# Kernel optimization log

Measured on AMD Instinct MI355X. Metric: run time of the kernel, lower is better.

The kernel has to match this reference:

```python
import jax, jax.numpy as jnp
import numpy as np

N_NODES = 100000
N_EDGES = 1600000
N_GRAPHS = 1024
D = 128
L = 3
BN_EPS = 1e-5


def setup_inputs() -> dict:
    key = jax.random.key(0)
    ks = jax.random.split(key, 16)
    x = jax.random.normal(ks[0], (N_NODES, D), dtype=jnp.float32)
    edge_index = jax.random.randint(ks[1], (2, N_EDGES), 0, N_NODES, dtype=jnp.int64)
    batch = jnp.sort(jax.random.randint(ks[2], (N_NODES,), 0, N_GRAPHS, dtype=jnp.int64))
    w = lambda k, shape: jax.random.normal(k, shape, dtype=jnp.float32) * 0.05
    return {
        "x": x,
        "edge_index": edge_index,
        "batch": batch,
        "conv_W1": w(ks[3], (L, D, D)),
        "conv_b1": w(ks[4], (L, D)),
        "bn_gamma": jax.random.uniform(ks[5], (L, D), dtype=jnp.float32) + 0.5,
        "bn_beta": w(ks[6], (L, D)),
        "bn_mean": w(ks[7], (L, D)),
        "bn_var": jax.random.uniform(ks[8], (L, D), dtype=jnp.float32) + 0.5,
        "conv_W2": w(ks[9], (L, D, D)),
        "conv_b2": w(ks[10], (L, D)),
        "head_W1": w(ks[11], (D, D)),
        "head_b1": w(ks[12], (D,)),
        "head_W2": w(ks[13], (D, D)),
        "head_b2": w(ks[14], (D,)),
    }


def reference(x, edge_index, batch, conv_W1, conv_b1, bn_gamma, bn_beta,
              bn_mean, bn_var, conv_W2, conv_b2, head_W1, head_b1,
              head_W2, head_b2):
    n = x.shape[0]
    src, dst = edge_index[0], edge_index[1]
    for l in range(L):
        # GINConv, eps=0: nn(x + sum_{j->i} x_j)
        agg = jax.ops.segment_sum(x[src], dst, num_segments=n)  # [N, D]
        h = x + agg
        # MLP([in, h, h]): Linear -> BatchNorm(eval) -> ReLU -> Linear
        h = h @ conv_W1[l] + conv_b1[l]
        h = (h - bn_mean[l]) * jax.lax.rsqrt(bn_var[l] + BN_EPS) * bn_gamma[l] + bn_beta[l]
        h = jax.nn.relu(h)
        h = h @ conv_W2[l] + conv_b2[l]
        x = jax.nn.relu(h)  # .relu() in the outer forward
    # global_add_pool over graph ids
    g = jax.ops.segment_sum(x, batch, num_segments=N_GRAPHS)  # [B, D]
    # head MLP (norm=None, dropout inactive at eval): Linear -> ReLU -> Linear
    g = jax.nn.relu(g @ head_W1 + head_b1)
    return g @ head_W2 + head_b2
```

## Files before the change

### kernel.cpp

```cpp
#include <hip/hip_runtime.h>

#define N_NODES  100000
#define N_EDGES  1600000
#define N_GRAPHS 1024
#define D        128
#define BN_EPS   1e-5f

#define FNSLICE      98
#define FSLICE_NODES 1024
#define FSLICE_CAP   20480
#define QCAP         96
#define CCHUNK       4000
#define CGRID        400

#define CVT_BLOCKS   6250
#define PW_BLOCKS    384
#define FOLD_BLOCKS  3
#define PZ_BLOCKS    128
#define PZ_BASE      (CVT_BLOCKS + PW_BLOCKS + FOLD_BLOCKS)
#define MISC_BASE    (PZ_BASE + PZ_BLOCKS)
#define COMPACT_BASE (MISC_BASE + 1)
#define SETUP_GRID   (COMPACT_BASE + CGRID)

#define GATHER_GRID  12500

typedef short bf16x8 __attribute__((ext_vector_type(8)));
typedef float f32x4  __attribute__((ext_vector_type(4)));

__device__ __forceinline__ ushort f2bf(float f) {
    unsigned int b = __float_as_uint(f);
    return (ushort)((b + 0x7fffu + ((b >> 16) & 1u)) >> 16);
}
__device__ __forceinline__ float bflo(unsigned int u) { return __uint_as_float(u << 16); }
__device__ __forceinline__ float bfhi(unsigned int u) { return __uint_as_float(u & 0xffff0000u); }
__device__ __forceinline__ unsigned int packbf(float x, float y) {
    return (unsigned int)f2bf(x) | ((unsigned int)f2bf(y) << 16);
}

__global__ __launch_bounds__(256) void setup_kernel(
        const float* __restrict__ x, ushort* __restrict__ xb,
        const float* __restrict__ W1, const float* __restrict__ W2,
        ushort* __restrict__ Wt,
        const float* __restrict__ b1, const float* __restrict__ gamma,
        const float* __restrict__ beta, const float* __restrict__ mean,
        const float* __restrict__ var, const float* __restrict__ b2,
        float* __restrict__ folds, float* __restrict__ pool,
        int* __restrict__ slice_tail, int* __restrict__ offsets,
        const int* __restrict__ src, const int* __restrict__ dst,
        unsigned int* __restrict__ squeue) {
    __shared__ unsigned int qbuf[FNSLICE * QCAP];
    __shared__ int qcnt[FNSLICE];
    __shared__ int qbase[FNSLICE];
    int b = blockIdx.x, t = threadIdx.x;
    if (b < CVT_BLOCKS) {
        size_t i = ((size_t)b * 256 + t) * 8;
        float4 v0 = *(const float4*)(x + i);
        float4 v1 = *(const float4*)(x + i + 4);
        uint4 o;
        o.x = packbf(v0.x, v0.y); o.y = packbf(v0.z, v0.w);
        o.z = packbf(v1.x, v1.y); o.w = packbf(v1.z, v1.w);
        *(uint4*)(xb + i) = o;
    } else if (b < CVT_BLOCKS + PW_BLOCKS) {
        int idx = (b - CVT_BLOCKS) * 256 + t;
        int i = idx >> 14, r = idx & 16383;
        int n = r >> 7, k = r & 127, l = i >> 1;
        const float* W = (i & 1) ? (W2 + (size_t)l * D * D) : (W1 + (size_t)l * D * D);
        Wt[idx] = f2bf(W[k * D + n]);
    } else if (b < PZ_BASE) {
        int idx = (b - CVT_BLOCKS - PW_BLOCKS) * 256 + t;
        if (idx < 6 * D) {
            int i = idx >> 7, j = idx & 127, l = i >> 1;
            float s, o;
            if ((i & 1) == 0) {
                float sv = gamma[l * D + j] * rsqrtf(var[l * D + j] + BN_EPS);
                s = sv;
                o = (b1[l * D + j] - mean[l * D + j]) * sv + beta[l * D + j];
            } else {
                s = 1.0f;
                o = b2[l * D + j];
            }
            folds[(size_t)i * 2 * D + j]     = s;
            folds[(size_t)i * 2 * D + D + j] = o;
        }
    } else if (b < MISC_BASE) {
        int idx = (b - PZ_BASE) * 256 + t;
        ((float4*)pool)[idx] = float4{0.f, 0.f, 0.f, 0.f};
    } else if (b == MISC_BASE) {
        if (t == 255) offsets[N_NODES] = N_EDGES;
    } else {
        for (int i = t; i < FNSLICE; i += 256) qcnt[i] = 0;
        __syncthreads();
        int e0 = (b - COMPACT_BASE) * CCHUNK;
        int eend = e0 + CCHUNK; if (eend > N_EDGES) eend = N_EDGES;
        for (int e = e0 + t; e < eend; e += 256) {
            int d = dst[e], s = src[e];
            int sl = d >> 10;
            unsigned int pk = ((unsigned int)(d & 1023) << 17) | (unsigned int)s;
            int pos = atomicAdd(&qcnt[sl], 1);
            if (pos < QCAP) qbuf[sl * QCAP + pos] = pk;
            else {
                int gp = atomicAdd(&slice_tail[sl], 1);
                squeue[(size_t)sl * FSLICE_CAP + gp] = pk;
            }
        }
        __syncthreads();
        for (int i = t; i < FNSLICE; i += 256) {
            int n = qcnt[i]; if (n > QCAP) n = QCAP;
            qbase[i] = atomicAdd(&slice_tail[i], n);
        }
        __syncthreads();
        int wv = t >> 6, ln = t & 63;
        for (int sl = wv; sl < FNSLICE; sl += 4) {
            int n = qcnt[sl]; if (n > QCAP) n = QCAP;
            int gb = qbase[sl];
            for (int i = ln; i < n; i += 64)
                squeue[(size_t)sl * FSLICE_CAP + gb + i] = qbuf[sl * QCAP + i];
        }
    }
}

__global__ __launch_bounds__(1024) void fill_local(const unsigned int* __restrict__ squeue,
                                                   const int* __restrict__ slice_tail,
                                                   int* __restrict__ offsets,
                                                   int* __restrict__ csr_src) {
    __shared__ int hist[FSLICE_NODES];
    __shared__ int cur[FSLICE_NODES];
    __shared__ int sbase[128];
    __shared__ int wsum[16];
    int sl = blockIdx.x, t = threadIdx.x;
    int n = slice_tail[sl];
    if (t < 128) sbase[t] = (t < FNSLICE) ? slice_tail[t] : 0;
    hist[t] = 0;
    __syncthreads();
    for (int off = 1; off < 128; off <<= 1) {
        int u = (t < 128 && t >= off) ? sbase[t - off] : 0;
        __syncthreads();
        if (t < 128) sbase[t] += u;
        __syncthreads();
    }
    int gbase = (sl == 0) ? 0 : sbase[sl - 1];
    size_t qb = (size_t)sl * FSLICE_CAP;
    for (int i = t; i < n; i += 1024)
        atomicAdd(&hist[squeue[qb + i] >> 17], 1);
    __syncthreads();
    int c = hist[t];
    int lane = t & 63, w = t >> 6;
    int sc = c;
#pragma unroll
    for (int off = 1; off < 64; off <<= 1) {
        int u = __shfl_up(sc, off, 64);
        if (lane >= off) sc += u;
    }
    if (lane == 63) wsum[w] = sc;
    __syncthreads();
    if (t < 16) {
        int ws = wsum[t];
        int s2 = ws;
#pragma unroll
        for (int off = 1; off < 16; off <<= 1) {
            int u = __shfl_up(s2, off, 16);
            if (t >= off) s2 += u;
        }
        wsum[t] = s2 - ws;
    }
    __syncthreads();
    int gslot = gbase + sc + wsum[w] - c;
    cur[t] = gslot;
    int node = sl * FSLICE_NODES + t;
    if (node < N_NODES) offsets[node] = gslot;
    __syncthreads();
    for (int i = t; i < n; i += 1024) {
        unsigned int p = squeue[qb + i];
        int slot = atomicAdd(&cur[p >> 17], 1);
        csr_src[slot] = (int)(p & 0x1FFFFu);
    }
}

__device__ __forceinline__ void drain_stream(const unsigned int* __restrict__ base,
                                             const int* __restrict__ csr,
                                             int i, int e, int lane,
                                             float& ax, float& ay) {
    for (; i + 15 < e; i += 16) {
        int s0 = csr[i],      s1 = csr[i + 1],  s2 = csr[i + 2],  s3 = csr[i + 3];
        int s4 = csr[i + 4],  s5 = csr[i + 5],  s6 = csr[i + 6],  s7 = csr[i + 7];
        int s8 = csr[i + 8],  s9 = csr[i + 9],  sa = csr[i + 10], sb = csr[i + 11];
        int sc = csr[i + 12], sd = csr[i + 13], se = csr[i + 14], sf = csr[i + 15];
        unsigned int v0 = base[(size_t)s0 * 64 + lane];
        unsigned int v1 = base[(size_t)s1 * 64 + lane];
        unsigned int v2 = base[(size_t)s2 * 64 + lane];
        unsigned int v3 = base[(size_t)s3 * 64 + lane];
        unsigned int v4 = base[(size_t)s4 * 64 + lane];
        unsigned int v5 = base[(size_t)s5 * 64 + lane];
        unsigned int v6 = base[(size_t)s6 * 64 + lane];
        unsigned int v7 = base[(size_t)s7 * 64 + lane];
        unsigned int v8 = base[(size_t)s8 * 64 + lane];
        unsigned int v9 = base[(size_t)s9 * 64 + lane];
        unsigned int va = base[(size_t)sa * 64 + lane];
        unsigned int vb = base[(size_t)sb * 64 + lane];
        unsigned int vc = base[(size_t)sc * 64 + lane];
        unsigned int vd = base[(size_t)sd * 64 + lane];
        unsigned int ve = base[(size_t)se * 64 + lane];
        unsigned int vf = base[(size_t)sf * 64 + lane];
        ax += bflo(v0) + bflo(v1) + bflo(v2) + bflo(v3)
            + bflo(v4) + bflo(v5) + bflo(v6) + bflo(v7)
            + bflo(v8) + bflo(v9) + bflo(va) + bflo(vb)
            + bflo(vc) + bflo(vd) + bflo(ve) + bflo(vf);
        ay += bfhi(v0) + bfhi(v1) + bfhi(v2) + bfhi(v3)
            + bfhi(v4) + bfhi(v5) + bfhi(v6) + bfhi(v7)
            + bfhi(v8) + bfhi(v9) + bfhi(va) + bfhi(vb)
            + bfhi(vc) + bfhi(vd) + bfhi(ve) + bfhi(vf);
    }
    for (; i + 3 < e; i += 4) {
        int s0 = csr[i], s1 = csr[i + 1], s2 = csr[i + 2], s3 = csr[i + 3];
        unsigned int v0 = base[(size_t)s0 * 64 + lane];
        unsigned int v1 = base[(size_t)s1 * 64 + lane];
        unsigned int v2 = base[(size_t)s2 * 64 + lane];
        unsigned int v3 = base[(size_t)s3 * 64 + lane];
        ax += bflo(v0) + bflo(v1) + bflo(v2) + bflo(v3);
        ay += bfhi(v0) + bfhi(v1) + bfhi(v2) + bfhi(v3);
    }
    for (; i < e; ++i) {
        unsigned int v = base[(size_t)csr[i] * 64 + lane];
        ax += bflo(v); ay += bfhi(v);
    }
}

__global__ __launch_bounds__(256) void gather_bf16(const ushort* __restrict__ xb,
                                                   const int* __restrict__ offsets,
                                                   const int* __restrict__ csr_src,
                                                   ushort* __restrict__ hb) {
    int wv = threadIdx.x >> 6, lane = threadIdx.x & 63;
    int n0 = (blockIdx.x * 4 + wv) * 2;
    const unsigned int* base = (const unsigned int*)xb;
    unsigned int u0 = base[(size_t)n0 * 64 + lane];
    unsigned int u1 = base[(size_t)(n0 + 1) * 64 + lane];
    float ax0 = bflo(u0), ay0 = bfhi(u0);
    float ax1 = bflo(u1), ay1 = bfhi(u1);
    int i0 = offsets[n0];
    int e0 = offsets[n0 + 1];
    int i1 = e0;
    int e1 = offsets[n0 + 2];
    while (i0 + 7 < e0 && i1 + 7 < e1) {
        int s0 = csr_src[i0],     s1 = csr_src[i0 + 1],
            s2 = csr_src[i0 + 2], s3 = csr_src[i0 + 3];
        int s4 = csr_src[i0 + 4], s5 = csr_src[i0 + 5],
            s6 = csr_src[i0 + 6], s7 = csr_src[i0 + 7];
        int r0 = csr_src[i1],     r1 = csr_src[i1 + 1],
            r2 = csr_src[i1 + 2], r3 = csr_src[i1 + 3];
        int r4 = csr_src[i1 + 4], r5 = csr_src[i1 + 5],
            r6 = csr_src[i1 + 6], r7 = csr_src[i1 + 7];
        unsigned int v0 = base[(size_t)s0 * 64 + lane];
        unsigned int v1 = base[(size_t)s1 * 64 + lane];
        unsigned int v2 = base[(size_t)s2 * 64 + lane];
        unsigned int v3 = base[(size_t)s3 * 64 + lane];
        unsigned int v4 = base[(size_t)s4 * 64 + lane];
        unsigned int v5 = base[(size_t)s5 * 64 + lane];
        unsigned int v6 = base[(size_t)s6 * 64 + lane];
        unsigned int v7 = base[(size_t)s7 * 64 + lane];
        unsigned int w0 = base[(size_t)r0 * 64 + lane];
        unsigned int w1 = base[(size_t)r1 * 64 + lane];
        unsigned int w2 = base[(size_t)r2 * 64 + lane];
        unsigned int w3 = base[(size_t)r3 * 64 + lane];
        unsigned int w4 = base[(size_t)r4 * 64 + lane];
        unsigned int w5 = base[(size_t)r5 * 64 + lane];
        unsigned int w6 = base[(size_t)r6 * 64 + lane];
        unsigned int w7 = base[(size_t)r7 * 64 + lane];
        ax0 += bflo(v0) + bflo(v1) + bflo(v2) + bflo(v3)
             + bflo(v4) + bflo(v5) + bflo(v6) + bflo(v7);
        ay0 += bfhi(v0) + bfhi(v1) + bfhi(v2) + bfhi(v3)
             + bfhi(v4) + bfhi(v5) + bfhi(v6) + bfhi(v7);
        ax1 += bflo(w0) + bflo(w1) + bflo(w2) + bflo(w3)
             + bflo(w4) + bflo(w5) + bflo(w6) + bflo(w7);
        ay1 += bfhi(w0) + bfhi(w1) + bfhi(w2) + bfhi(w3)
             + bfhi(w4) + bfhi(w5) + bfhi(w6) + bfhi(w7);
        i0 += 8; i1 += 8;
    }
    drain_stream(base, csr_src, i0, e0, lane, ax0, ay0);
    drain_stream(base, csr_src, i1, e1, lane, ax1, ay1);
    ((unsigned int*)hb)[(size_t)n0 * 64 + lane]       = packbf(ax0, ay0);
    ((unsigned int*)hb)[(size_t)(n0 + 1) * 64 + lane] = packbf(ax1, ay1);
}

__global__ __launch_bounds__(512, 4) void fused_gemm(const ushort* __restrict__ in,
                                                     ushort* __restrict__ out,
                                                     const ushort* __restrict__ Wt1,
                                                     const ushort* __restrict__ Wt2,
                                                     const float* __restrict__ fold1,
                                                     const float* __restrict__ fold2) {
    __shared__ ushort As[128 * 136];
    __shared__ ushort Bs[128 * 136];
    int t = threadIdx.x;
    int row0 = blockIdx.x * 128;

#pragma unroll
    for (int i = 0; i < 4; ++i) {
        int f = t + 512 * i; int m = f >> 4, g = f & 15;
        *(float4*)(As + m * 136 + g * 8) = *(const float4*)(in + (size_t)(row0 + m) * D + g * 8);
        *(float4*)(Bs + m * 136 + g * 8) = *(const float4*)(Wt1 + (size_t)m * D + g * 8);
    }
    const uint4* w2v = (const uint4*)Wt2;
    uint4 p0 = w2v[t];
    uint4 p1 = w2v[t + 512];
    uint4 p2 = w2v[t + 1024];
    uint4 p3 = w2v[t + 1536];
    __syncthreads();

    int lane = t & 63, wv = t >> 6;
    int quad = lane >> 4, mr = lane & 15;
    int mbase = wv * 16;
    const ushort* ap = As + (mbase + mr) * 136 + quad * 8;
    bf16x8 a0 = *(const bf16x8*)(ap);
    bf16x8 a1 = *(const bf16x8*)(ap + 32);
    bf16x8 a2 = *(const bf16x8*)(ap + 64);
    bf16x8 a3 = *(const bf16x8*)(ap + 96);

#pragma unroll
    for (int nt = 0; nt < 8; ++nt) {
        const ushort* bq = Bs + (nt * 16 + mr) * 136 + quad * 8;
        bf16x8 b0 = *(const bf16x8*)(bq);
        bf16x8 b1 = *(const bf16x8*)(bq + 32);
        bf16x8 b2 = *(const bf16x8*)(bq + 64);
        bf16x8 b3 = *(const bf16x8*)(bq + 96);
        f32x4 acc = {0.f, 0.f, 0.f, 0.f};
        acc = __builtin_amdgcn_mfma_f32_16x16x32_bf16(a0, b0, acc, 0, 0, 0);
        acc = __builtin_amdgcn_mfma_f32_16x16x32_bf16(a1, b1, acc, 0, 0, 0);
        acc = __builtin_amdgcn_mfma_f32_16x16x32_bf16(a2, b2, acc, 0, 0, 0);
        acc = __builtin_amdgcn_mfma_f32_16x16x32_bf16(a3, b3, acc, 0, 0, 0);
        int j = nt * 16 + mr;
        float s = fold1[j], o = fold1[D + j];
#pragma unroll
        for (int r = 0; r < 4; ++r) {
            float z = fmaxf(fmaf(acc[r], s, o), 0.0f);
            As[(mbase + quad * 4 + r) * 136 + j] = f2bf(z);
        }
    }
    __syncthreads();

    {
        int f0 = t;          *(uint4*)(Bs + (f0 >> 4) * 136 + (f0 & 15) * 8) = p0;
        int f1 = t + 512;    *(uint4*)(Bs + (f1 >> 4) * 136 + (f1 & 15) * 8) = p1;
        int f2 = t + 1024;   *(uint4*)(Bs + (f2 >> 4) * 136 + (f2 & 15) * 8) = p2;
        int f3 = t + 1536;   *(uint4*)(Bs + (f3 >> 4) * 136 + (f3 & 15) * 8) = p3;
    }
    const ushort* hp = As + (mbase + mr) * 136 + quad * 8;
    bf16x8 h0 = *(const bf16x8*)(hp);
    bf16x8 h1 = *(const bf16x8*)(hp + 32);
    bf16x8 h2 = *(const bf16x8*)(hp + 64);
    bf16x8 h3 = *(const bf16x8*)(hp + 96);
    __syncthreads();

#pragma unroll
    for (int nt = 0; nt < 8; ++nt) {
        const ushort* bq = Bs + (nt * 16 + mr) * 136 + quad * 8;
        bf16x8 b0 = *(const bf16x8*)(bq);
        bf16x8 b1 = *(const bf16x8*)(bq + 32);
        bf16x8 b2 = *(const bf16x8*)(bq + 64);
        bf16x8 b3 = *(const bf16x8*)(bq + 96);
        f32x4 acc = {0.f, 0.f, 0.f, 0.f};
        acc = __builtin_amdgcn_mfma_f32_16x16x32_bf16(h0, b0, acc, 0, 0, 0);
        acc = __builtin_amdgcn_mfma_f32_16x16x32_bf16(h1, b1, acc, 0, 0, 0);
        acc = __builtin_amdgcn_mfma_f32_16x16x32_bf16(h2, b2, acc, 0, 0, 0);
        acc = __builtin_amdgcn_mfma_f32_16x16x32_bf16(h3, b3, acc, 0, 0, 0);
        int j = nt * 16 + mr;
        float o = fold2[D + j];
#pragma unroll
        for (int r = 0; r < 4; ++r) {
            float z = fmaxf(acc[r] + o, 0.0f);
            As[(mbase + quad * 4 + r) * 136 + j] = f2bf(z);
        }
    }
    __syncthreads();

#pragma unroll
    for (int i = 0; i < 8; ++i) {
        int f = t + 512 * i; int lr = f >> 5, g = f & 31;
        if (row0 + lr < N_NODES)
            *(float2*)(out + (size_t)(row0 + lr) * D + g * 4) =
                *(const float2*)(As + lr * 136 + g * 4);
    }
}

__global__ __launch_bounds__(512, 4) void fused_gemm_pool(const ushort* __restrict__ in,
                                                          const int* __restrict__ batch,
                                                          float* __restrict__ pool,
                                                          const ushort* __restrict__ Wt1,
                                                          const ushort* __restrict__ Wt2,
                                                          const float* __restrict__ fold1,
                                                          const float* __restrict__ fold2) {
    __shared__ ushort As[128 * 136];
    __shared__ ushort Bs[128 * 136];
    __shared__ int bb[128];
    int t = threadIdx.x;
    int row0 = blockIdx.x * 128;

#pragma unroll
    for (int i = 0; i < 4; ++i) {
        int f = t + 512 * i; int m = f >> 4, g = f & 15;
        *(float4*)(As + m * 136 + g * 8) = *(const float4*)(in + (size_t)(row0 + m) * D + g * 8);
        *(float4*)(Bs + m * 136 + g * 8) = *(const float4*)(Wt1 + (size_t)m * D + g * 8);
    }
    const uint4* w2v = (const uint4*)Wt2;
    uint4 p0 = w2v[t];
    uint4 p1 = w2v[t + 512];
    uint4 p2 = w2v[t + 1024];
    uint4 p3 = w2v[t + 1536];
    __syncthreads();

    int lane = t & 63, wv = t >> 6;
    int quad = lane >> 4, mr = lane & 15;
    int mbase = wv * 16;
    const ushort* ap = As + (mbase + mr) * 136 + quad * 8;
    bf16x8 a0 = *(const bf16x8*)(ap);
    bf16x8 a1 = *(const bf16x8*)(ap + 32);
    bf16x8 a2 = *(const bf16x8*)(ap + 64);
    bf16x8 a3 = *(const bf16x8*)(ap + 96);

#pragma unroll
    for (int nt = 0; nt < 8; ++nt) {
        const ushort* bq = Bs + (nt * 16 + mr) * 136 + quad * 8;
        bf16x8 b0 = *(const bf16x8*)(bq);
        bf16x8 b1 = *(const bf16x8*)(bq + 32);
        bf16x8 b2 = *(const bf16x8*)(bq + 64);
        bf16x8 b3 = *(const bf16x8*)(bq + 96);
        f32x4 acc = {0.f, 0.f, 0.f, 0.f};
        acc = __builtin_amdgcn_mfma_f32_16x16x32_bf16(a0, b0, acc, 0, 0, 0);
        acc = __builtin_amdgcn_mfma_f32_16x16x32_bf16(a1, b1, acc, 0, 0, 0);
        acc = __builtin_amdgcn_mfma_f32_16x16x32_bf16(a2, b2, acc, 0, 0, 0);
        acc = __builtin_amdgcn_mfma_f32_16x16x32_bf16(a3, b3, acc, 0, 0, 0);
        int j = nt * 16 + mr;
        float s = fold1[j], o = fold1[D + j];
#pragma unroll
        for (int r = 0; r < 4; ++r) {
            float z = fmaxf(fmaf(acc[r], s, o), 0.0f);
            As[(mbase + quad * 4 + r) * 136 + j] = f2bf(z);
        }
    }
    __syncthreads();

    {
        int f0 = t;          *(uint4*)(Bs + (f0 >> 4) * 136 + (f0 & 15) * 8) = p0;
        int f1 = t + 512;    *(uint4*)(Bs + (f1 >> 4) * 136 + (f1 & 15) * 8) = p1;
        int f2 = t + 1024;   *(uint4*)(Bs + (f2 >> 4) * 136 + (f2 & 15) * 8) = p2;
        int f3 = t + 1536;   *(uint4*)(Bs + (f3 >> 4) * 136 + (f3 & 15) * 8) = p3;
    }
    const ushort* hp = As + (mbase + mr) * 136 + quad * 8;
    bf16x8 h0 = *(const bf16x8*)(hp);
    bf16x8 h1 = *(const bf16x8*)(hp + 32);
    bf16x8 h2 = *(const bf16x8*)(hp + 64);
    bf16x8 h3 = *(const bf16x8*)(hp + 96);
    __syncthreads();

#pragma unroll
    for (int nt = 0; nt < 8; ++nt) {
        const ushort* bq = Bs + (nt * 16 + mr) * 136 + quad * 8;
        bf16x8 b0 = *(const bf16x8*)(bq);
        bf16x8 b1 = *(const bf16x8*)(bq + 32);
        bf16x8 b2 = *(const bf16x8*)(bq + 64);
        bf16x8 b3 = *(const bf16x8*)(bq + 96);
        f32x4 acc = {0.f, 0.f, 0.f, 0.f};
        acc = __builtin_amdgcn_mfma_f32_16x16x32_bf16(h0, b0, acc, 0, 0, 0);
        acc = __builtin_amdgcn_mfma_f32_16x16x32_bf16(h1, b1, acc, 0, 0, 0);
        acc = __builtin_amdgcn_mfma_f32_16x16x32_bf16(h2, b2, acc, 0, 0, 0);
        acc = __builtin_amdgcn_mfma_f32_16x16x32_bf16(h3, b3, acc, 0, 0, 0);
        int j = nt * 16 + mr;
        float o = fold2[D + j];
#pragma unroll
        for (int r = 0; r < 4; ++r) {
            float z = fmaxf(acc[r] + o, 0.0f);
            As[(mbase + quad * 4 + r) * 136 + j] = f2bf(z);
        }
    }
    if (t < 128)
        bb[t] = (row0 + t < N_NODES) ? batch[row0 + t] : -1;
    __syncthreads();

    {
        int j = t & 127, rg = t >> 7;
        int rbeg = rg * 32;
        if (row0 + rbeg < N_NODES) {
            int curg = bb[rbeg];
            float s = 0.0f;
#pragma unroll 1
            for (int r = rbeg; r < rbeg + 32; ++r) {
                if (row0 + r >= N_NODES) break;
                int g = bb[r];
                if (g != curg) {
                    atomicAdd(pool + (size_t)curg * D + j, s);
                    s = 0.0f; curg = g;
                }
                s += __uint_as_float((unsigned int)As[r * 136 + j] << 16);
            }
            atomicAdd(pool + (size_t)curg * D + j, s);
        }
    }
}

__global__ __launch_bounds__(128) void head_kernel(const float* __restrict__ pool,
                                                   const float* __restrict__ W1,
                                                   const float* __restrict__ b1,
                                                   const float* __restrict__ W2,
                                                   const float* __restrict__ b2,
                                                   float* __restrict__ out) {
    __shared__ float row[128];
    __shared__ float t1[128];
    int r = blockIdx.x, j = threadIdx.x;
    row[j] = pool[(size_t)r * D + j];
    __syncthreads();
    float a1 = b1[j];
    for (int k = 0; k < D; ++k) a1 = fmaf(row[k], W1[k * D + j], a1);
    t1[j] = fmaxf(a1, 0.0f);
    __syncthreads();
    float a2 = b2[j];
    for (int k = 0; k < D; ++k) a2 = fmaf(t1[k], W2[k * D + j], a2);
    out[r * D + j] = a2;
}

extern "C" void kernel_launch(void* const* d_in, const int* in_sizes, int n_in,
                              void* d_out, int out_size, void* d_ws, size_t ws_size,
                              hipStream_t stream) {
    const float* x        = (const float*)d_in[0];
    const int*   ei       = (const int*)d_in[1];
    const int*   src      = ei;
    const int*   dst      = ei + N_EDGES;
    const int*   batch    = (const int*)d_in[2];
    const float* conv_W1  = (const float*)d_in[3];
    const float* conv_b1  = (const float*)d_in[4];
    const float* bn_gamma = (const float*)d_in[5];
    const float* bn_beta  = (const float*)d_in[6];
    const float* bn_mean  = (const float*)d_in[7];
    const float* bn_var   = (const float*)d_in[8];
    const float* conv_W2  = (const float*)d_in[9];
    const float* conv_b2  = (const float*)d_in[10];
    const float* head_W1  = (const float*)d_in[11];
    const float* head_b1  = (const float*)d_in[12];
    const float* head_W2  = (const float*)d_in[13];
    const float* head_b2  = (const float*)d_in[14];
    float* out = (float*)d_out;

    char* ws = (char*)d_ws;
    size_t off = 0;
    auto alloc = [&](size_t bytes) -> void* {
        void* p = ws + off;
        off = (off + bytes + 255) & ~(size_t)255;
        return p;
    };
    const size_t NODE_BUF = (size_t)(N_NODES + 128) * D * sizeof(ushort);
    ushort* buf0    = (ushort*)alloc(NODE_BUF);
    ushort* buf1    = (ushort*)alloc(NODE_BUF);
    ushort* Wt      = (ushort*)alloc((size_t)6 * D * D * sizeof(ushort));
    float*  folds   = (float*)alloc((size_t)6 * 2 * D * sizeof(float));
    unsigned int* squeue = (unsigned int*)alloc((size_t)FNSLICE * FSLICE_CAP * sizeof(unsigned int));
    int*   csr_src  = (int*)alloc((size_t)(N_EDGES + 64) * sizeof(int));
    int*   offsets  = (int*)alloc((size_t)(N_NODES + 1) * sizeof(int));
    int*   slice_tail = (int*)alloc((size_t)FNSLICE * sizeof(int));
    float* pool     = (float*)alloc((size_t)N_GRAPHS * D * sizeof(float));

    hipMemsetAsync(slice_tail, 0, FNSLICE * sizeof(int), stream);
    setup_kernel<<<SETUP_GRID, 256, 0, stream>>>(
        x, buf0, conv_W1, conv_W2, Wt,
        conv_b1, bn_gamma, bn_beta, bn_mean, bn_var, conv_b2, folds, pool,
        slice_tail, offsets, src, dst, squeue);
    fill_local<<<FNSLICE, 1024, 0, stream>>>(squeue, slice_tail, offsets, csr_src);

    const int FUSED_GRID = (N_NODES + 127) / 128;
    for (int l = 0; l < 2; ++l) {
        gather_bf16<<<GATHER_GRID, 256, 0, stream>>>(buf0, offsets, csr_src, buf1);
        fused_gemm<<<FUSED_GRID, 512, 0, stream>>>(buf1, buf0,
            Wt + (size_t)(2 * l) * D * D, Wt + (size_t)(2 * l + 1) * D * D,
            folds + (size_t)(2 * l) * 2 * D, folds + (size_t)(2 * l + 1) * 2 * D);
    }
    gather_bf16<<<GATHER_GRID, 256, 0, stream>>>(buf0, offsets, csr_src, buf1);
    fused_gemm_pool<<<FUSED_GRID, 512, 0, stream>>>(buf1, batch, pool,
        Wt + (size_t)4 * D * D, Wt + (size_t)5 * D * D,
        folds + (size_t)4 * 2 * D, folds + (size_t)5 * 2 * D);

    head_kernel<<<N_GRAPHS, 128, 0, stream>>>(pool, head_W1, head_b1,
                                              head_W2, head_b2, out);
}
```

Measured before the change: 411.4 us.

## Halve fused GEMM row tile to 64 and split output columns across waves

The fused two-layer MLP kernels now handle 64 rows per block instead of 128. The 8 waves are split into 4 row bands times 2 column halves, so each wave computes 4 of the 8 output column tiles. This doubles the block count, shrinks LDS per block and raises the occupancy hint from 4 to 6, aiming for better latency hiding and fewer idle CUs. The cost is loading the full weight matrices twice as often per row and adding an extra barrier. The pool tail check now relies on the -1 sentinel instead of a bounds compare.

```diff
diff --git a/kernel.cpp b/kernel.cpp
--- a/kernel.cpp
+++ b/kernel.cpp
@@ -23,6 +23,7 @@
 #define SETUP_GRID   (COMPACT_BASE + CGRID)
 
 #define GATHER_GRID  12500
+#define N_TILES      1563
 
 typedef short bf16x8 __attribute__((ext_vector_type(8)));
 typedef float f32x4  __attribute__((ext_vector_type(4)));
@@ -281,21 +282,25 @@
     ((unsigned int*)hb)[(size_t)(n0 + 1) * 64 + lane] = packbf(ax1, ay1);
 }
 
-__global__ __launch_bounds__(512, 4) void fused_gemm(const ushort* __restrict__ in,
+__global__ __launch_bounds__(512, 6) void fused_gemm(const ushort* __restrict__ in,
                                                      ushort* __restrict__ out,
                                                      const ushort* __restrict__ Wt1,
                                                      const ushort* __restrict__ Wt2,
                                                      const float* __restrict__ fold1,
                                                      const float* __restrict__ fold2) {
-    __shared__ ushort As[128 * 136];
+    __shared__ ushort As[64 * 136];
     __shared__ ushort Bs[128 * 136];
     int t = threadIdx.x;
-    int row0 = blockIdx.x * 128;
-
+    int row0 = blockIdx.x * 64;
+
+#pragma unroll
+    for (int i = 0; i < 2; ++i) {
+        int f = t + 512 * i; int m = f >> 4, g = f & 15;
+        *(float4*)(As + m * 136 + g * 8) = *(const float4*)(in + (size_t)(row0 + m) * D + g * 8);
+    }
 #pragma unroll
     for (int i = 0; i < 4; ++i) {
         int f = t + 512 * i; int m = f >> 4, g = f & 15;
-        *(float4*)(As + m * 136 + g * 8) = *(const float4*)(in + (size_t)(row0 + m) * D + g * 8);
         *(float4*)(Bs + m * 136 + g * 8) = *(const float4*)(Wt1 + (size_t)m * D + g * 8);
     }
     const uint4* w2v = (const uint4*)Wt2;
@@ -307,15 +312,18 @@
 
     int lane = t & 63, wv = t >> 6;
     int quad = lane >> 4, mr = lane & 15;
-    int mbase = wv * 16;
-    const ushort* ap = As + (mbase + mr) * 136 + quad * 8;
+    int rb = wv & 3, ch = wv >> 2;
+    int rbase = rb * 16;
+    const ushort* ap = As + (rbase + mr) * 136 + quad * 8;
     bf16x8 a0 = *(const bf16x8*)(ap);
     bf16x8 a1 = *(const bf16x8*)(ap + 32);
     bf16x8 a2 = *(const bf16x8*)(ap + 64);
     bf16x8 a3 = *(const bf16x8*)(ap + 96);
-
-#pragma unroll
-    for (int nt = 0; nt < 8; ++nt) {
+    __syncthreads();
+
+#pragma unroll
+    for (int nt4 = 0; nt4 < 4; ++nt4) {
+        int nt = ch * 4 + nt4;
         const ushort* bq = Bs + (nt * 16 + mr) * 136 + quad * 8;
         bf16x8 b0 = *(const bf16x8*)(bq);
         bf16x8 b1 = *(const bf16x8*)(bq + 32);
@@ -331,7 +339,7 @@
 #pragma unroll
         for (int r = 0; r < 4; ++r) {
             float z = fmaxf(fmaf(acc[r], s, o), 0.0f);
-            As[(mbase + quad * 4 + r) * 136 + j] = f2bf(z);
+            As[(rbase + quad * 4 + r) * 136 + j] = f2bf(z);
         }
     }
     __syncthreads();
@@ -342,7 +350,7 @@
         int f2 = t + 1024;   *(uint4*)(Bs + (f2 >> 4) * 136 + (f2 & 15) * 8) = p2;
         int f3 = t + 1536;   *(uint4*)(Bs + (f3 >> 4) * 136 + (f3 & 15) * 8) = p3;
     }
-    const ushort* hp = As + (mbase + mr) * 136 + quad * 8;
+    const ushort* hp = As + (rbase + mr) * 136 + quad * 8;
     bf16x8 h0 = *(const bf16x8*)(hp);
     bf16x8 h1 = *(const bf16x8*)(hp + 32);
     bf16x8 h2 = *(const bf16x8*)(hp + 64);
@@ -350,7 +358,8 @@
     __syncthreads();
 
 #pragma unroll
-    for (int nt = 0; nt < 8; ++nt) {
+    for (int nt4 = 0; nt4 < 4; ++nt4) {
+        int nt = ch * 4 + nt4;
         const ushort* bq = Bs + (nt * 16 + mr) * 136 + quad * 8;
         bf16x8 b0 = *(const bf16x8*)(bq);
         bf16x8 b1 = *(const bf16x8*)(bq + 32);
@@ -366,13 +375,13 @@
 #pragma unroll
         for (int r = 0; r < 4; ++r) {
             float z = fmaxf(acc[r] + o, 0.0f);
-            As[(mbase + quad * 4 + r) * 136 + j] = f2bf(z);
-        }
-    }
-    __syncthreads();
-
-#pragma unroll
-    for (int i = 0; i < 8; ++i) {
+            As[(rbase + quad * 4 + r) * 136 + j] = f2bf(z);
+        }
+    }
+    __syncthreads();
+
+#pragma unroll
+    for (int i = 0; i < 4; ++i) {
         int f = t + 512 * i; int lr = f >> 5, g = f & 31;
         if (row0 + lr < N_NODES)
             *(float2*)(out + (size_t)(row0 + lr) * D + g * 4) =
@@ -380,23 +389,27 @@
     }
 }
 
-__global__ __launch_bounds__(512, 4) void fused_gemm_pool(const ushort* __restrict__ in,
+__global__ __launch_bounds__(512, 6) void fused_gemm_pool(const ushort* __restrict__ in,
                                                           const int* __restrict__ batch,
                                                           float* __restrict__ pool,
                                                           const ushort* __restrict__ Wt1,
                                                           const ushort* __restrict__ Wt2,
                                                           const float* __restrict__ fold1,
                                                           const float* __restrict__ fold2) {
-    __shared__ ushort As[128 * 136];
+    __shared__ ushort As[64 * 136];
     __shared__ ushort Bs[128 * 136];
-    __shared__ int bb[128];
+    __shared__ int bb[64];
     int t = threadIdx.x;
-    int row0 = blockIdx.x * 128;
-
+    int row0 = blockIdx.x * 64;
+
+#pragma unroll
+    for (int i = 0; i < 2; ++i) {
+        int f = t + 512 * i; int m = f >> 4, g = f & 15;
+        *(float4*)(As + m * 136 + g * 8) = *(const float4*)(in + (size_t)(row0 + m) * D + g * 8);
+    }
 #pragma unroll
     for (int i = 0; i < 4; ++i) {
         int f = t + 512 * i; int m = f >> 4, g = f & 15;
-        *(float4*)(As + m * 136 + g * 8) = *(const float4*)(in + (size_t)(row0 + m) * D + g * 8);
         *(float4*)(Bs + m * 136 + g * 8) = *(const float4*)(Wt1 + (size_t)m * D + g * 8);
     }
     const uint4* w2v = (const uint4*)Wt2;
@@ -408,15 +421,18 @@
 
     int lane = t & 63, wv = t >> 6;
     int quad = lane >> 4, mr = lane & 15;
-    int mbase = wv * 16;
-    const ushort* ap = As + (mbase + mr) * 136 + quad * 8;
+    int rb = wv & 3, ch = wv >> 2;
+    int rbase = rb * 16;
+    const ushort* ap = As + (rbase + mr) * 136 + quad * 8;
     bf16x8 a0 = *(const bf16x8*)(ap);
     bf16x8 a1 = *(const bf16x8*)(ap + 32);
     bf16x8 a2 = *(const bf16x8*)(ap + 64);
     bf16x8 a3 = *(const bf16x8*)(ap + 96);
-
-#pragma unroll
-    for (int nt = 0; nt < 8; ++nt) {
+    __syncthreads();
+
+#pragma unroll
+    for (int nt4 = 0; nt4 < 4; ++nt4) {
+        int nt = ch * 4 + nt4;
         const ushort* bq = Bs + (nt * 16 + mr) * 136 + quad * 8;
         bf16x8 b0 = *(const bf16x8*)(bq);
         bf16x8 b1 = *(const bf16x8*)(bq + 32);
@@ -432,7 +448,7 @@
 #pragma unroll
         for (int r = 0; r < 4; ++r) {
             float z = fmaxf(fmaf(acc[r], s, o), 0.0f);
-            As[(mbase + quad * 4 + r) * 136 + j] = f2bf(z);
+            As[(rbase + quad * 4 + r) * 136 + j] = f2bf(z);
         }
     }
     __syncthreads();
@@ -443,7 +459,7 @@
         int f2 = t + 1024;   *(uint4*)(Bs + (f2 >> 4) * 136 + (f2 & 15) * 8) = p2;
         int f3 = t + 1536;   *(uint4*)(Bs + (f3 >> 4) * 136 + (f3 & 15) * 8) = p3;
     }
-    const ushort* hp = As + (mbase + mr) * 136 + quad * 8;
+    const ushort* hp = As + (rbase + mr) * 136 + quad * 8;
     bf16x8 h0 = *(const bf16x8*)(hp);
     bf16x8 h1 = *(const bf16x8*)(hp + 32);
     bf16x8 h2 = *(const bf16x8*)(hp + 64);
@@ -451,7 +467,8 @@
     __syncthreads();
 
 #pragma unroll
-    for (int nt = 0; nt < 8; ++nt) {
+    for (int nt4 = 0; nt4 < 4; ++nt4) {
+        int nt = ch * 4 + nt4;
         const ushort* bq = Bs + (nt * 16 + mr) * 136 + quad * 8;
         bf16x8 b0 = *(const bf16x8*)(bq);
         bf16x8 b1 = *(const bf16x8*)(bq + 32);
@@ -467,23 +484,23 @@
 #pragma unroll
         for (int r = 0; r < 4; ++r) {
             float z = fmaxf(acc[r] + o, 0.0f);
-            As[(mbase + quad * 4 + r) * 136 + j] = f2bf(z);
-        }
-    }
-    if (t < 128)
+            As[(rbase + quad * 4 + r) * 136 + j] = f2bf(z);
+        }
+    }
+    if (t < 64)
         bb[t] = (row0 + t < N_NODES) ? batch[row0 + t] : -1;
     __syncthreads();
 
     {
         int j = t & 127, rg = t >> 7;
-        int rbeg = rg * 32;
+        int rbeg = rg * 16;
         if (row0 + rbeg < N_NODES) {
             int curg = bb[rbeg];
             float s = 0.0f;
 #pragma unroll 1
-            for (int r = rbeg; r < rbeg + 32; ++r) {
-                if (row0 + r >= N_NODES) break;
+            for (int r = rbeg; r < rbeg + 16; ++r) {
                 int g = bb[r];
+                if (g < 0) break;
                 if (g != curg) {
                     atomicAdd(pool + (size_t)curg * D + j, s);
                     s = 0.0f; curg = g;
@@ -562,15 +579,14 @@
         slice_tail, offsets, src, dst, squeue);
     fill_local<<<FNSLICE, 1024, 0, stream>>>(squeue, slice_tail, offsets, csr_src);
 
-    const int FUSED_GRID = (N_NODES + 127) / 128;
     for (int l = 0; l < 2; ++l) {
         gather_bf16<<<GATHER_GRID, 256, 0, stream>>>(buf0, offsets, csr_src, buf1);
-        fused_gemm<<<FUSED_GRID, 512, 0, stream>>>(buf1, buf0,
+        fused_gemm<<<N_TILES, 512, 0, stream>>>(buf1, buf0,
             Wt + (size_t)(2 * l) * D * D, Wt + (size_t)(2 * l + 1) * D * D,
             folds + (size_t)(2 * l) * 2 * D, folds + (size_t)(2 * l + 1) * 2 * D);
     }
     gather_bf16<<<GATHER_GRID, 256, 0, stream>>>(buf0, offsets, csr_src, buf1);
-    fused_gemm_pool<<<FUSED_GRID, 512, 0, stream>>>(buf1, batch, pool,
+    fused_gemm_pool<<<N_TILES, 512, 0, stream>>>(buf1, batch, pool,
         Wt + (size_t)4 * D * D, Wt + (size_t)5 * D * D,
         folds + (size_t)4 * 2 * D, folds + (size_t)5 * 2 * D);
 
```

New measurement: 409.3 us (median of 2 runs). No clear change (-0.5%).
